# Performance work log

Hardware: AMD Instinct MI355X
Metric: run time of the kernel (lower is better)

## Reference

```python
import jax, jax.numpy as jnp
import numpy as np

N_NODES = 50000

def setup_inputs() -> dict:
    key = jax.random.key(0)
    ks = jax.random.split(key, 8)
    d_in, d_h = 128, 128
    x = jax.random.normal(ks[0], (N_NODES, d_in), dtype=jnp.float32)
    edge_index = jax.random.randint(ks[1], (2, 800000), 0, N_NODES, dtype=jnp.int64)
    edge_pairs = jax.random.randint(ks[2], (1000000, 2), 0, N_NODES, dtype=jnp.int64)
    W_gcn = jax.random.normal(ks[3], (d_in, d_h), dtype=jnp.float32) / np.sqrt(d_in)
    b_gcn = jnp.zeros((d_h,), dtype=jnp.float32)
    W1 = jax.random.normal(ks[4], (2 * d_h, d_h), dtype=jnp.float32) / np.sqrt(2 * d_h)
    b1 = jnp.zeros((d_h,), dtype=jnp.float32)
    W2 = jax.random.normal(ks[5], (d_h, 1), dtype=jnp.float32) / np.sqrt(d_h)
    b2 = jnp.zeros((1,), dtype=jnp.float32)
    return {"x": x, "edge_index": edge_index, "edge_pairs": edge_pairs,
            "W_gcn": W_gcn, "b_gcn": b_gcn, "W1": W1, "b1": b1, "W2": W2, "b2": b2}

def gcn_conv(x, edge_index, W, b):
    # PyG GCNConv default: add self-loops, symmetric normalization.
    n = x.shape[0]
    loop = jnp.arange(n, dtype=edge_index.dtype)
    src = jnp.concatenate([edge_index[0], loop])  # [E+N]
    dst = jnp.concatenate([edge_index[1], loop])
    deg = jax.ops.segment_sum(jnp.ones(src.shape[0], dtype=x.dtype), dst, num_segments=n)
    dinv = jnp.where(deg > 0, jax.lax.rsqrt(deg), 0.0)
    norm = dinv[src] * dinv[dst]                  # [E+N]
    h = x @ W                                     # [N, H]
    agg = jax.ops.segment_sum(h[src] * norm[:, None], dst, num_segments=n)
    return agg + b

def reference(x, edge_index, edge_pairs, W_gcn, b_gcn, W1, b1, W2, b2):
    h = gcn_conv(x, edge_index, W_gcn, b_gcn)      # [N, H]
    e = jnp.concatenate([h[edge_pairs[:, 0]], h[edge_pairs[:, 1]]], axis=-1)  # [P, 2H]
    edge_logits = jax.nn.relu(e @ W1 + b1) @ W2 + b2  # [P, 1]
    return edge_logits, edge_pairs, h
```

## Files before the change

### kernel.cpp

```cpp
#include <hip/hip_runtime.h>
#include <hip/hip_fp16.h>

#define WG 256

typedef _Float16 f16;
typedef _Float16 hv2 __attribute__((ext_vector_type(2)));
typedef _Float16 f16x4 __attribute__((ext_vector_type(4)));
typedef _Float16 f16x8 __attribute__((ext_vector_type(8)));
typedef float f32x4 __attribute__((ext_vector_type(4)));

__global__ __launch_bounds__(WG) void k_deg_count(const int* __restrict__ dst,
                                                  int* __restrict__ deg,
                                                  int* __restrict__ rank, int e) {
    int i = blockIdx.x * WG + threadIdx.x;
    if (i < e) rank[i] = atomicAdd(&deg[dst[i]], 1);
}

__global__ __launch_bounds__(WG) void k_scan1(const int* __restrict__ deg,
                                              float* __restrict__ dinv,
                                              int* __restrict__ base,
                                              int* __restrict__ bsum, int n) {
    __shared__ int t[WG];
    int tid = threadIdx.x;
    int i = blockIdx.x * WG + tid;
    int v = (i < n) ? deg[i] : 0;
    if (i < n) dinv[i] = rsqrtf((float)(v + 1));
    t[tid] = v;
    __syncthreads();
    for (int o = 1; o < WG; o <<= 1) {
        int add = (tid >= o) ? t[tid - o] : 0;
        __syncthreads();
        t[tid] += add;
        __syncthreads();
    }
    if (i < n) base[i] = t[tid] - v;
    if (tid == WG - 1) bsum[blockIdx.x] = t[WG - 1];
}

__global__ __launch_bounds__(WG) void k_scan23(int* __restrict__ base,
                                               const int* __restrict__ bsum,
                                               int n, int e, int nb) {
    __shared__ int t[WG];
    int tid = threadIdx.x;
    int v = (tid < nb) ? bsum[tid] : 0;
    t[tid] = v;
    __syncthreads();
    for (int o = 1; o < WG; o <<= 1) {
        int add = (tid >= o) ? t[tid - o] : 0;
        __syncthreads();
        t[tid] += add;
        __syncthreads();
    }
    int off = t[blockIdx.x] - ((blockIdx.x < nb) ? bsum[blockIdx.x] : 0);
    int i = blockIdx.x * WG + tid;
    if (i < n) {
        base[i] += off;
        if (i == n - 1) base[n] = e;
    }
}

__global__ __launch_bounds__(WG) void k_fill(const int* __restrict__ src,
                                             const int* __restrict__ dst,
                                             const int* __restrict__ base,
                                             const int* __restrict__ rank,
                                             int* __restrict__ esrc, int e) {
    int i = blockIdx.x * WG + threadIdx.x;
    if (i >= e) return;
    esrc[base[dst[i]] + rank[i]] = src[i];
}

__global__ __launch_bounds__(WG) void k_misc(const float* __restrict__ Wg,
                                             f16* __restrict__ Wgt,
                                             const float* __restrict__ W1,
                                             f16* __restrict__ W1t,
                                             const int* __restrict__ pairs,
                                             float* __restrict__ outp, int n4) {
    int b = blockIdx.x;
    if (b < 64) {
        int i = b * WG + threadIdx.x;
        int k = i & 127, nI = i >> 7;
        Wgt[i] = (f16)Wg[(size_t)k * 128 + nI];
    } else if (b < 192) {
        int i = (b - 64) * WG + threadIdx.x;
        int k = i & 255, nI = i >> 8;
        W1t[i] = (f16)W1[(size_t)k * 128 + nI];
    } else {
        int i = (b - 192) * WG + threadIdx.x;
        if (i < n4) {
            int4 v = ((const int4*)pairs)[i];
            ((float4*)outp)[i] = make_float4((float)v.x, (float)v.y, (float)v.z, (float)v.w);
        }
    }
}

__global__ __launch_bounds__(WG) void k_mm_hpk(const float* __restrict__ A,
                                               const f16* __restrict__ Wt,
                                               const float* __restrict__ dinv,
                                               __half2* __restrict__ Out, int n) {
    __shared__ f16 As[64][136];
    __shared__ f16 Bs[128][136];
    const int tid = threadIdx.x;
    const int row0 = blockIdx.x * 64;
    for (int f = tid; f < 128 * 16; f += WG) {
        int r = f >> 4, c = f & 15;
        *(float4*)&Bs[r][c * 8] = ((const float4*)Wt)[r * 16 + c];
    }
    for (int f = tid; f < 64 * 32; f += WG) {
        int r = f >> 5, c = f & 31;
        float4 v = make_float4(0.f, 0.f, 0.f, 0.f);
        if (row0 + r < n) v = ((const float4*)A)[(size_t)(row0 + r) * 32 + c];
        *(f16x4*)&As[r][c * 4] = (f16x4){(f16)v.x, (f16)v.y, (f16)v.z, (f16)v.w};
    }
    __syncthreads();
    const int wv = tid >> 6, lane = tid & 63, m = lane & 15, quad = lane >> 4;
    f32x4 acc[8];
#pragma unroll
    for (int t = 0; t < 8; ++t) acc[t] = (f32x4){0.f, 0.f, 0.f, 0.f};
#pragma unroll
    for (int kk = 0; kk < 4; ++kk) {
        f16x8 af = *(f16x8*)&As[wv * 16 + m][kk * 32 + quad * 8];
#pragma unroll
        for (int t = 0; t < 8; ++t) {
            f16x8 bf = *(f16x8*)&Bs[t * 16 + m][kk * 32 + quad * 8];
            acc[t] = __builtin_amdgcn_mfma_f32_16x16x32_f16(af, bf, acc[t], 0, 0, 0);
        }
    }
#pragma unroll
    for (int r = 0; r < 4; ++r) {
        int row = row0 + wv * 16 + quad * 4 + r;
        if (row < n) {
            float dv = dinv[row];
#pragma unroll
            for (int t = 0; t < 4; ++t)
                Out[(size_t)row * 64 + t * 16 + m] =
                    __floats2half2_rn(acc[t][r] * dv, acc[t + 4][r] * dv);
        }
    }
}

__global__ __launch_bounds__(WG) void k_mm_uv(const float* __restrict__ A,
                                              const f16* __restrict__ W1t,
                                              const float* __restrict__ b1,
                                              __half2* __restrict__ Up,
                                              __half2* __restrict__ Vp, int n) {
    __shared__ f16 As[64][136];
    __shared__ f16 Bs[128][136];
    const int tid = threadIdx.x;
    const int row0 = blockIdx.x * 64;
    for (int f = tid; f < 64 * 32; f += WG) {
        int r = f >> 5, c = f & 31;
        float4 v = make_float4(0.f, 0.f, 0.f, 0.f);
        if (row0 + r < n) v = ((const float4*)A)[(size_t)(row0 + r) * 32 + c];
        *(f16x4*)&As[r][c * 4] = (f16x4){(f16)v.x, (f16)v.y, (f16)v.z, (f16)v.w};
    }
    const int wv = tid >> 6, lane = tid & 63, m = lane & 15, quad = lane >> 4;
    f32x4 acc[8];
#pragma unroll
    for (int ph = 0; ph < 2; ++ph) {
        if (ph) __syncthreads();
        for (int f = tid; f < 128 * 16; f += WG) {
            int r = f >> 4, c = f & 15;
            *(float4*)&Bs[r][c * 8] = *(const float4*)(W1t + (size_t)r * 256 + ph * 128 + c * 8);
        }
        __syncthreads();
#pragma unroll
        for (int t = 0; t < 8; ++t) acc[t] = (f32x4){0.f, 0.f, 0.f, 0.f};
#pragma unroll
        for (int kk = 0; kk < 4; ++kk) {
            f16x8 af = *(f16x8*)&As[wv * 16 + m][kk * 32 + quad * 8];
#pragma unroll
            for (int t = 0; t < 8; ++t) {
                f16x8 bf = *(f16x8*)&Bs[t * 16 + m][kk * 32 + quad * 8];
                acc[t] = __builtin_amdgcn_mfma_f32_16x16x32_f16(af, bf, acc[t], 0, 0, 0);
            }
        }
        __half2* Out = ph ? Vp : Up;
#pragma unroll
        for (int t = 0; t < 4; ++t) {
            float bl = 0.f, bh = 0.f;
            if (!ph) { bl = b1[t * 16 + m]; bh = b1[t * 16 + m + 64]; }
#pragma unroll
            for (int r = 0; r < 4; ++r) {
                int row = row0 + wv * 16 + quad * 4 + r;
                if (row < n)
                    Out[(size_t)row * 64 + t * 16 + m] =
                        __floats2half2_rn(acc[t][r] + bl, acc[t + 4][r] + bh);
            }
        }
    }
}

__global__ __launch_bounds__(WG) void k_gather(const __half2* __restrict__ Hpk,
                                               const float* __restrict__ dinv,
                                               const float* __restrict__ bg,
                                               const int* __restrict__ base,
                                               const int* __restrict__ esrc,
                                               float* __restrict__ outh, int n) {
    int tid = threadIdx.x;
    int node = blockIdx.x * 16 + (tid >> 4);
    int sub = tid & 15;
    if (node >= n) return;
    int4 hh = *(const int4*)(Hpk + (size_t)node * 64 + 4 * sub);
    const int* hp = (const int*)&hh;
    float accl[4], acch[4];
#pragma unroll
    for (int k = 0; k < 4; ++k) {
        hv2 h = __builtin_bit_cast(hv2, hp[k]);
        accl[k] = (float)h[0];
        acch[k] = (float)h[1];
    }
    int j = base[node], jend = base[node + 1];
    for (; j + 4 <= jend; j += 4) {
        int s0 = esrc[j], s1 = esrc[j + 1], s2i = esrc[j + 2], s3 = esrc[j + 3];
        int4 r0 = *(const int4*)(Hpk + (size_t)s0 * 64 + 4 * sub);
        int4 r1 = *(const int4*)(Hpk + (size_t)s1 * 64 + 4 * sub);
        int4 r2 = *(const int4*)(Hpk + (size_t)s2i * 64 + 4 * sub);
        int4 r3 = *(const int4*)(Hpk + (size_t)s3 * 64 + 4 * sub);
        const int* p0 = (const int*)&r0;
        const int* p1 = (const int*)&r1;
        const int* p2 = (const int*)&r2;
        const int* p3 = (const int*)&r3;
#pragma unroll
        for (int k = 0; k < 4; ++k) {
            hv2 h0 = __builtin_bit_cast(hv2, p0[k]);
            hv2 h1 = __builtin_bit_cast(hv2, p1[k]);
            hv2 h2 = __builtin_bit_cast(hv2, p2[k]);
            hv2 h3 = __builtin_bit_cast(hv2, p3[k]);
            accl[k] += (float)h0[0] + (float)h1[0] + (float)h2[0] + (float)h3[0];
            acch[k] += (float)h0[1] + (float)h1[1] + (float)h2[1] + (float)h3[1];
        }
    }
    for (; j < jend; ++j) {
        int s = esrc[j];
        int4 r = *(const int4*)(Hpk + (size_t)s * 64 + 4 * sub);
        const int* pr = (const int*)&r;
#pragma unroll
        for (int k = 0; k < 4; ++k) {
            hv2 h = __builtin_bit_cast(hv2, pr[k]);
            accl[k] += (float)h[0];
            acch[k] += (float)h[1];
        }
    }
    float dv = dinv[node];
    float4 blo = *(const float4*)(bg + 4 * sub);
    float4 bhi = *(const float4*)(bg + 4 * sub + 64);
    *(float4*)&outh[(size_t)node * 128 + 4 * sub] =
        make_float4(fmaf(accl[0], dv, blo.x), fmaf(accl[1], dv, blo.y),
                    fmaf(accl[2], dv, blo.z), fmaf(accl[3], dv, blo.w));
    *(float4*)&outh[(size_t)node * 128 + 64 + 4 * sub] =
        make_float4(fmaf(acch[0], dv, bhi.x), fmaf(acch[1], dv, bhi.y),
                    fmaf(acch[2], dv, bhi.z), fmaf(acch[3], dv, bhi.w));
}

__global__ __launch_bounds__(WG) void k_pair8(const __half2* __restrict__ U,
                                              const __half2* __restrict__ V,
                                              const float* __restrict__ W2,
                                              const float* __restrict__ b2,
                                              const int* __restrict__ pairs,
                                              float* __restrict__ out_logit, int p) {
    int wv = (blockIdx.x * WG + threadIdx.x) >> 6;
    int lane = threadIdx.x & 63;
    int g = lane >> 4, sub = lane & 15;
    int q0 = wv * 8 + g, q1 = q0 + 4;
    bool v0 = (q0 < p), v1 = (q1 < p);
    if (!v0) return;
    int qa0 = q0, qa1 = v1 ? q1 : q0;
    int a0 = pairs[2 * qa0], b0 = pairs[2 * qa0 + 1];
    int a1 = pairs[2 * qa1], b1i = pairs[2 * qa1 + 1];

    float4 w2lo = ((const float4*)W2)[sub];
    float4 w2hi = ((const float4*)(W2 + 64))[sub];
    hv2 w2h[4];
    w2h[0] = hv2{(f16)w2lo.x, (f16)w2hi.x};
    w2h[1] = hv2{(f16)w2lo.y, (f16)w2hi.y};
    w2h[2] = hv2{(f16)w2lo.z, (f16)w2hi.z};
    w2h[3] = hv2{(f16)w2lo.w, (f16)w2hi.w};

    int4 u0 = *(const int4*)(U + (size_t)a0 * 64 + 4 * sub);
    int4 vv0 = *(const int4*)(V + (size_t)b0 * 64 + 4 * sub);
    int4 u1 = *(const int4*)(U + (size_t)a1 * 64 + 4 * sub);
    int4 vv1 = *(const int4*)(V + (size_t)b1i * 64 + 4 * sub);
    const int* ui0 = (const int*)&u0;
    const int* vi0 = (const int*)&vv0;
    const int* ui1 = (const int*)&u1;
    const int* vi1 = (const int*)&vv1;

    const hv2 z2 = hv2{(f16)0.f, (f16)0.f};
    float p0 = 0.f, p1 = 0.f;
#pragma unroll
    for (int k = 0; k < 4; ++k) {
        hv2 s0 = __builtin_bit_cast(hv2, ui0[k]) + __builtin_bit_cast(hv2, vi0[k]);
        hv2 s1 = __builtin_bit_cast(hv2, ui1[k]) + __builtin_bit_cast(hv2, vi1[k]);
        p0 = __builtin_amdgcn_fdot2(__builtin_elementwise_max(s0, z2), w2h[k], p0, false);
        p1 = __builtin_amdgcn_fdot2(__builtin_elementwise_max(s1, z2), w2h[k], p1, false);
    }
#pragma unroll
    for (int m = 1; m < 16; m <<= 1) {
        p0 += __shfl_xor(p0, m, 64);
        p1 += __shfl_xor(p1, m, 64);
    }
    if (sub == 0) {
        float bb = b2[0];
        out_logit[q0] = p0 + bb;
        if (v1) out_logit[q1] = p1 + bb;
    }
}

extern "C" void kernel_launch(void* const* d_in, const int* in_sizes, int n_in,
                              void* d_out, int out_size, void* d_ws, size_t ws_size,
                              hipStream_t stream) {
    const float* x     = (const float*)d_in[0];
    const int*   eidx  = (const int*)d_in[1];
    const int*   pairs = (const int*)d_in[2];
    const float* W_gcn = (const float*)d_in[3];
    const float* b_gcn = (const float*)d_in[4];
    const float* W1    = (const float*)d_in[5];
    const float* b1    = (const float*)d_in[6];
    const float* W2    = (const float*)d_in[7];
    const float* b2    = (const float*)d_in[8];

    const int N = in_sizes[0] / 128;
    const int E = in_sizes[1] / 2;
    const int P = in_sizes[2] / 2;
    const int* esrc_in = eidx;
    const int* edst_in = eidx + E;

    float* ws      = (float*)d_ws;
    int*   deg     = (int*)d_ws;
    float* dinv    = ws + 65536;
    int*   base    = (int*)(ws + 131072);
    int*   bsum    = (int*)(ws + 196608);
    f16*   Wt_gcn  = (f16*)(ws + 197120);
    f16*   W1t     = (f16*)(ws + 205312);
    int*   rank    = (int*)(ws + 221696);
    int*   ecsr    = (int*)(ws + 221696 + (size_t)E);
    __half2* Hpk   = (__half2*)(ws + 221696 + 2 * (size_t)E);
    __half2* Upk   = Hpk + (size_t)N * 64;
    __half2* Vpk   = Upk + (size_t)N * 64;

    float* out_logit = (float*)d_out;
    float* out_pairs = out_logit + P;
    float* out_h     = out_logit + 3 * (size_t)P;

    const int nb = (N + WG - 1) / WG;
    dim3 blk(WG);
    dim3 grid_pair((unsigned)((P + 31) / 32));
    dim3 grid_misc((unsigned)(192 + (P / 2 + WG - 1) / WG));
    hipMemsetAsync(deg, 0, (size_t)N * 4, stream);
    k_deg_count <<<(E + WG - 1) / WG, blk, 0, stream>>>(edst_in, deg, rank, E);
    k_scan1     <<<nb, blk, 0, stream>>>(deg, dinv, base, bsum, N);
    k_scan23    <<<nb, blk, 0, stream>>>(base, bsum, N, E, nb);
    k_fill      <<<(E + WG - 1) / WG, blk, 0, stream>>>(esrc_in, edst_in, base, rank, ecsr, E);
    k_misc      <<<grid_misc, blk, 0, stream>>>(W_gcn, Wt_gcn, W1, W1t, pairs, out_pairs, P / 2);
    k_mm_hpk    <<<(N + 63) / 64, blk, 0, stream>>>(x, Wt_gcn, dinv, Hpk, N);
    k_gather    <<<(N + 15) / 16, blk, 0, stream>>>(Hpk, dinv, b_gcn, base, ecsr, out_h, N);
    k_mm_uv     <<<(N + 63) / 64, blk, 0, stream>>>(out_h, W1t, b1, Upk, Vpk, N);
    k_pair8     <<<grid_pair, blk, 0, stream>>>(Upk, Vpk, W2, b2, pairs, out_logit, P);
}
```

Baseline: 280.0 us.

## Bucket edge pairs by source node to reuse U rows in pair scoring

New measurement: 317.2 us. 1.13x slower.

```diff
diff --git a/kernel.cpp b/kernel.cpp
--- a/kernel.cpp
+++ b/kernel.cpp
@@ -9,22 +9,40 @@
 typedef _Float16 f16x8 __attribute__((ext_vector_type(8)));
 typedef float f32x4 __attribute__((ext_vector_type(4)));
 
-__global__ __launch_bounds__(WG) void k_deg_count(const int* __restrict__ dst,
-                                                  int* __restrict__ deg,
-                                                  int* __restrict__ rank, int e) {
+__global__ __launch_bounds__(WG) void k_count2(const int* __restrict__ dst,
+                                               int* __restrict__ deg,
+                                               int* __restrict__ rank,
+                                               const int* __restrict__ pairs,
+                                               int* __restrict__ pdeg,
+                                               int* __restrict__ prank,
+                                               int e, int p) {
     int i = blockIdx.x * WG + threadIdx.x;
-    if (i < e) rank[i] = atomicAdd(&deg[dst[i]], 1);
-}
-
-__global__ __launch_bounds__(WG) void k_scan1(const int* __restrict__ deg,
-                                              float* __restrict__ dinv,
-                                              int* __restrict__ base,
-                                              int* __restrict__ bsum, int n) {
+    if (i < e) {
+        rank[i] = atomicAdd(&deg[dst[i]], 1);
+    } else if (i < e + p) {
+        int j = i - e;
+        prank[j] = atomicAdd(&pdeg[pairs[2 * j]], 1);
+    }
+}
+
+__global__ __launch_bounds__(WG) void k_scan1x2(const int* __restrict__ deg,
+                                                float* __restrict__ dinv,
+                                                int* __restrict__ base,
+                                                int* __restrict__ bsum,
+                                                const int* __restrict__ pdeg,
+                                                int* __restrict__ pbase,
+                                                int* __restrict__ pbsum,
+                                                int n, int nb) {
     __shared__ int t[WG];
     int tid = threadIdx.x;
-    int i = blockIdx.x * WG + tid;
-    int v = (i < n) ? deg[i] : 0;
-    if (i < n) dinv[i] = rsqrtf((float)(v + 1));
+    bool second = (blockIdx.x >= (unsigned)nb);
+    int bid = second ? (blockIdx.x - nb) : blockIdx.x;
+    const int* src = second ? pdeg : deg;
+    int* dstb = second ? pbase : base;
+    int* bs = second ? pbsum : bsum;
+    int i = bid * WG + tid;
+    int v = (i < n) ? src[i] : 0;
+    if (!second && i < n) dinv[i] = rsqrtf((float)(v + 1));
     t[tid] = v;
     __syncthreads();
     for (int o = 1; o < WG; o <<= 1) {
@@ -33,16 +51,23 @@
         t[tid] += add;
         __syncthreads();
     }
-    if (i < n) base[i] = t[tid] - v;
-    if (tid == WG - 1) bsum[blockIdx.x] = t[WG - 1];
-}
-
-__global__ __launch_bounds__(WG) void k_scan23(int* __restrict__ base,
-                                               const int* __restrict__ bsum,
-                                               int n, int e, int nb) {
+    if (i < n) dstb[i] = t[tid] - v;
+    if (tid == WG - 1) bs[bid] = t[WG - 1];
+}
+
+__global__ __launch_bounds__(WG) void k_scan23x2(int* __restrict__ base,
+                                                 const int* __restrict__ bsum,
+                                                 int* __restrict__ pbase,
+                                                 const int* __restrict__ pbsum,
+                                                 int n, int e, int p, int nb) {
     __shared__ int t[WG];
     int tid = threadIdx.x;
-    int v = (tid < nb) ? bsum[tid] : 0;
+    bool second = (blockIdx.x >= (unsigned)nb);
+    int bid = second ? (blockIdx.x - nb) : blockIdx.x;
+    const int* bs = second ? pbsum : bsum;
+    int* dstb = second ? pbase : base;
+    int total = second ? p : e;
+    int v = (tid < nb) ? bs[tid] : 0;
     t[tid] = v;
     __syncthreads();
     for (int o = 1; o < WG; o <<= 1) {
@@ -51,22 +76,32 @@
         t[tid] += add;
         __syncthreads();
     }
-    int off = t[blockIdx.x] - ((blockIdx.x < nb) ? bsum[blockIdx.x] : 0);
-    int i = blockIdx.x * WG + tid;
+    int off = t[bid] - ((bid < nb) ? bs[bid] : 0);
+    int i = bid * WG + tid;
     if (i < n) {
-        base[i] += off;
-        if (i == n - 1) base[n] = e;
-    }
-}
-
-__global__ __launch_bounds__(WG) void k_fill(const int* __restrict__ src,
-                                             const int* __restrict__ dst,
-                                             const int* __restrict__ base,
-                                             const int* __restrict__ rank,
-                                             int* __restrict__ esrc, int e) {
+        dstb[i] += off;
+        if (i == n - 1) dstb[n] = total;
+    }
+}
+
+__global__ __launch_bounds__(WG) void k_fill2(const int* __restrict__ src,
+                                              const int* __restrict__ dst,
+                                              const int* __restrict__ base,
+                                              const int* __restrict__ rank,
+                                              int* __restrict__ esrc,
+                                              const int* __restrict__ pairs,
+                                              const int* __restrict__ pbase,
+                                              const int* __restrict__ prank,
+                                              int2* __restrict__ plist,
+                                              int e, int p) {
     int i = blockIdx.x * WG + threadIdx.x;
-    if (i >= e) return;
-    esrc[base[dst[i]] + rank[i]] = src[i];
+    if (i < e) {
+        esrc[base[dst[i]] + rank[i]] = src[i];
+    } else if (i < e + p) {
+        int j = i - e;
+        int a = pairs[2 * j], b = pairs[2 * j + 1];
+        plist[pbase[a] + prank[j]] = make_int2(b, j);
+    }
 }
 
 __global__ __launch_bounds__(WG) void k_misc(const float* __restrict__ Wg,
@@ -252,21 +287,22 @@
                     fmaf(acch[2], dv, bhi.z), fmaf(acch[3], dv, bhi.w));
 }
 
-__global__ __launch_bounds__(WG) void k_pair8(const __half2* __restrict__ U,
-                                              const __half2* __restrict__ V,
-                                              const float* __restrict__ W2,
-                                              const float* __restrict__ b2,
-                                              const int* __restrict__ pairs,
-                                              float* __restrict__ out_logit, int p) {
-    int wv = (blockIdx.x * WG + threadIdx.x) >> 6;
-    int lane = threadIdx.x & 63;
-    int g = lane >> 4, sub = lane & 15;
-    int q0 = wv * 8 + g, q1 = q0 + 4;
-    bool v0 = (q0 < p), v1 = (q1 < p);
-    if (!v0) return;
-    int qa0 = q0, qa1 = v1 ? q1 : q0;
-    int a0 = pairs[2 * qa0], b0 = pairs[2 * qa0 + 1];
-    int a1 = pairs[2 * qa1], b1i = pairs[2 * qa1 + 1];
+__global__ __launch_bounds__(WG) void k_pairs_csr(const __half2* __restrict__ U,
+                                                  const __half2* __restrict__ V,
+                                                  const float* __restrict__ W2,
+                                                  const float* __restrict__ b2,
+                                                  const int* __restrict__ pbase,
+                                                  const int2* __restrict__ plist,
+                                                  float* __restrict__ out_logit, int n) {
+    int tid = threadIdx.x;
+    int node = blockIdx.x * 16 + (tid >> 4);
+    int sub = tid & 15;
+    if (node >= n) return;
+    int j = pbase[node], jend = pbase[node + 1];
+    if (j >= jend) return;
+
+    int4 uu = *(const int4*)(U + (size_t)node * 64 + 4 * sub);
+    const int* ui = (const int*)&uu;
 
     float4 w2lo = ((const float4*)W2)[sub];
     float4 w2hi = ((const float4*)(W2 + 64))[sub];
@@ -275,34 +311,59 @@
     w2h[1] = hv2{(f16)w2lo.y, (f16)w2hi.y};
     w2h[2] = hv2{(f16)w2lo.z, (f16)w2hi.z};
     w2h[3] = hv2{(f16)w2lo.w, (f16)w2hi.w};
-
-    int4 u0 = *(const int4*)(U + (size_t)a0 * 64 + 4 * sub);
-    int4 vv0 = *(const int4*)(V + (size_t)b0 * 64 + 4 * sub);
-    int4 u1 = *(const int4*)(U + (size_t)a1 * 64 + 4 * sub);
-    int4 vv1 = *(const int4*)(V + (size_t)b1i * 64 + 4 * sub);
-    const int* ui0 = (const int*)&u0;
-    const int* vi0 = (const int*)&vv0;
-    const int* ui1 = (const int*)&u1;
-    const int* vi1 = (const int*)&vv1;
-
+    float bb = b2[0];
     const hv2 z2 = hv2{(f16)0.f, (f16)0.f};
-    float p0 = 0.f, p1 = 0.f;
-#pragma unroll
-    for (int k = 0; k < 4; ++k) {
-        hv2 s0 = __builtin_bit_cast(hv2, ui0[k]) + __builtin_bit_cast(hv2, vi0[k]);
-        hv2 s1 = __builtin_bit_cast(hv2, ui1[k]) + __builtin_bit_cast(hv2, vi1[k]);
-        p0 = __builtin_amdgcn_fdot2(__builtin_elementwise_max(s0, z2), w2h[k], p0, false);
-        p1 = __builtin_amdgcn_fdot2(__builtin_elementwise_max(s1, z2), w2h[k], p1, false);
-    }
-#pragma unroll
-    for (int m = 1; m < 16; m <<= 1) {
-        p0 += __shfl_xor(p0, m, 64);
-        p1 += __shfl_xor(p1, m, 64);
-    }
-    if (sub == 0) {
-        float bb = b2[0];
-        out_logit[q0] = p0 + bb;
-        if (v1) out_logit[q1] = p1 + bb;
+
+    for (; j + 4 <= jend; j += 4) {
+        int2 e0 = plist[j], e1 = plist[j + 1], e2 = plist[j + 2], e3 = plist[j + 3];
+        int4 v0 = *(const int4*)(V + (size_t)e0.x * 64 + 4 * sub);
+        int4 v1 = *(const int4*)(V + (size_t)e1.x * 64 + 4 * sub);
+        int4 v2 = *(const int4*)(V + (size_t)e2.x * 64 + 4 * sub);
+        int4 v3 = *(const int4*)(V + (size_t)e3.x * 64 + 4 * sub);
+        const int* vi0 = (const int*)&v0;
+        const int* vi1 = (const int*)&v1;
+        const int* vi2 = (const int*)&v2;
+        const int* vi3 = (const int*)&v3;
+        float p0 = 0.f, p1 = 0.f, p2 = 0.f, p3 = 0.f;
+#pragma unroll
+        for (int k = 0; k < 4; ++k) {
+            hv2 uk = __builtin_bit_cast(hv2, ui[k]);
+            hv2 s0 = uk + __builtin_bit_cast(hv2, vi0[k]);
+            hv2 s1 = uk + __builtin_bit_cast(hv2, vi1[k]);
+            hv2 s2 = uk + __builtin_bit_cast(hv2, vi2[k]);
+            hv2 s3 = uk + __builtin_bit_cast(hv2, vi3[k]);
+            p0 = __builtin_amdgcn_fdot2(__builtin_elementwise_max(s0, z2), w2h[k], p0, false);
+            p1 = __builtin_amdgcn_fdot2(__builtin_elementwise_max(s1, z2), w2h[k], p1, false);
+            p2 = __builtin_amdgcn_fdot2(__builtin_elementwise_max(s2, z2), w2h[k], p2, false);
+            p3 = __builtin_amdgcn_fdot2(__builtin_elementwise_max(s3, z2), w2h[k], p3, false);
+        }
+#pragma unroll
+        for (int m = 1; m < 16; m <<= 1) {
+            p0 += __shfl_xor(p0, m, 64);
+            p1 += __shfl_xor(p1, m, 64);
+            p2 += __shfl_xor(p2, m, 64);
+            p3 += __shfl_xor(p3, m, 64);
+        }
+        if (sub == 0) {
+            out_logit[e0.y] = p0 + bb;
+            out_logit[e1.y] = p1 + bb;
+            out_logit[e2.y] = p2 + bb;
+            out_logit[e3.y] = p3 + bb;
+        }
+    }
+    for (; j < jend; ++j) {
+        int2 e0 = plist[j];
+        int4 v0 = *(const int4*)(V + (size_t)e0.x * 64 + 4 * sub);
+        const int* vi0 = (const int*)&v0;
+        float p0 = 0.f;
+#pragma unroll
+        for (int k = 0; k < 4; ++k) {
+            hv2 s0 = __builtin_bit_cast(hv2, ui[k]) + __builtin_bit_cast(hv2, vi0[k]);
+            p0 = __builtin_amdgcn_fdot2(__builtin_elementwise_max(s0, z2), w2h[k], p0, false);
+        }
+#pragma unroll
+        for (int m = 1; m < 16; m <<= 1) p0 += __shfl_xor(p0, m, 64);
+        if (sub == 0) out_logit[e0.y] = p0 + bb;
     }
 }
 
@@ -327,16 +388,21 @@
 
     float* ws      = (float*)d_ws;
     int*   deg     = (int*)d_ws;
-    float* dinv    = ws + 65536;
-    int*   base    = (int*)(ws + 131072);
-    int*   bsum    = (int*)(ws + 196608);
-    f16*   Wt_gcn  = (f16*)(ws + 197120);
-    f16*   W1t     = (f16*)(ws + 205312);
-    int*   rank    = (int*)(ws + 221696);
-    int*   ecsr    = (int*)(ws + 221696 + (size_t)E);
-    __half2* Hpk   = (__half2*)(ws + 221696 + 2 * (size_t)E);
+    int*   pdeg    = (int*)d_ws + N;
+    float* dinv    = ws + 131072;
+    int*   base    = (int*)(ws + 196608);
+    int*   pbase   = (int*)(ws + 262144);
+    int*   bsum    = (int*)(ws + 327680);
+    int*   pbsum   = (int*)(ws + 327936);
+    f16*   Wt_gcn  = (f16*)(ws + 328192);
+    f16*   W1t     = (f16*)(ws + 336384);
+    int*   rank    = (int*)(ws + 352768);
+    int*   ecsr    = rank + (size_t)E;
+    __half2* Hpk   = (__half2*)(ecsr + (size_t)E);
+    int*   prank   = (int*)Hpk;
     __half2* Upk   = Hpk + (size_t)N * 64;
     __half2* Vpk   = Upk + (size_t)N * 64;
+    int2*  plist   = (int2*)(Vpk + (size_t)N * 64);
 
     float* out_logit = (float*)d_out;
     float* out_pairs = out_logit + P;
@@ -344,16 +410,17 @@
 
     const int nb = (N + WG - 1) / WG;
     dim3 blk(WG);
-    dim3 grid_pair((unsigned)((P + 31) / 32));
+    dim3 grid_cnt((unsigned)((E + P + WG - 1) / WG));
     dim3 grid_misc((unsigned)(192 + (P / 2 + WG - 1) / WG));
-    hipMemsetAsync(deg, 0, (size_t)N * 4, stream);
-    k_deg_count <<<(E + WG - 1) / WG, blk, 0, stream>>>(edst_in, deg, rank, E);
-    k_scan1     <<<nb, blk, 0, stream>>>(deg, dinv, base, bsum, N);
-    k_scan23    <<<nb, blk, 0, stream>>>(base, bsum, N, E, nb);
-    k_fill      <<<(E + WG - 1) / WG, blk, 0, stream>>>(esrc_in, edst_in, base, rank, ecsr, E);
+    hipMemsetAsync(deg, 0, (size_t)(2 * N) * 4, stream);
+    k_count2    <<<grid_cnt, blk, 0, stream>>>(edst_in, deg, rank, pairs, pdeg, prank, E, P);
+    k_scan1x2   <<<2 * nb, blk, 0, stream>>>(deg, dinv, base, bsum, pdeg, pbase, pbsum, N, nb);
+    k_scan23x2  <<<2 * nb, blk, 0, stream>>>(base, bsum, pbase, pbsum, N, E, P, nb);
+    k_fill2     <<<grid_cnt, blk, 0, stream>>>(esrc_in, edst_in, base, rank, ecsr,
+                                               pairs, pbase, prank, plist, E, P);
     k_misc      <<<grid_misc, blk, 0, stream>>>(W_gcn, Wt_gcn, W1, W1t, pairs, out_pairs, P / 2);
     k_mm_hpk    <<<(N + 63) / 64, blk, 0, stream>>>(x, Wt_gcn, dinv, Hpk, N);
     k_gather    <<<(N + 15) / 16, blk, 0, stream>>>(Hpk, dinv, b_gcn, base, ecsr, out_h, N);
     k_mm_uv     <<<(N + 63) / 64, blk, 0, stream>>>(out_h, W1t, b1, Upk, Vpk, N);
-    k_pair8     <<<grid_pair, blk, 0, stream>>>(Upk, Vpk, W2, b2, pairs, out_logit, P);
-}
+    k_pairs_csr <<<(N + 15) / 16, blk, 0, stream>>>(Upk, Vpk, W2, b2, pbase, plist, out_logit, N);
+}
```
